# Kernel tuning notes

Measured on AMD Instinct MI355X. Metric: run time of the kernel, lower is better.

Reference implementation:

```python
import jax, jax.numpy as jnp
import numpy as np

D_MODEL = 1024
NUM_HEADS = 16
HEAD_DIM = D_MODEL // NUM_HEADS  # 64


def setup_inputs() -> dict:
    key = jax.random.key(0)
    ks = jax.random.split(key, 9)
    s = 1.0 / np.sqrt(D_MODEL)
    return {
        "x": jax.random.normal(ks[0], (2, 2048, D_MODEL), dtype=jnp.float32),
        "Wq": jax.random.normal(ks[1], (D_MODEL, D_MODEL), dtype=jnp.float32) * s,
        "bq": jnp.zeros((D_MODEL,), dtype=jnp.float32),
        "Wk": jax.random.normal(ks[2], (D_MODEL, HEAD_DIM), dtype=jnp.float32) * s,
        "bk": jnp.zeros((HEAD_DIM,), dtype=jnp.float32),
        "Wv": jax.random.normal(ks[3], (D_MODEL, HEAD_DIM), dtype=jnp.float32) * s,
        "bv": jnp.zeros((HEAD_DIM,), dtype=jnp.float32),
        "Wo": jax.random.normal(ks[4], (D_MODEL, D_MODEL), dtype=jnp.float32) * s,
        "bo": jnp.zeros((D_MODEL,), dtype=jnp.float32),
    }


def reference(x, Wq, bq, Wk, bk, Wv, bv, Wo, bo):
    B, S, D = x.shape
    H, hd = NUM_HEADS, HEAD_DIM
    # Projections: Q has H heads, K/V a single shared head (MQA).
    Q = (x @ Wq + bq).reshape(B, S, H, hd).transpose(0, 2, 1, 3)  # [B,H,S,hd]
    K = x @ Wk + bk  # [B,S,hd]
    V = x @ Wv + bv  # [B,S,hd]
    # Shared-K/V attention: broadcast K across heads instead of expand().
    scores = jnp.einsum("bhqd,bkd->bhqk", Q, K) / np.sqrt(hd)  # [B,H,S,S]
    attn = jax.nn.softmax(scores, axis=-1)
    attended = jnp.einsum("bhqk,bkd->bhqd", attn, V)  # [B,H,S,hd]
    attended = attended.transpose(0, 2, 1, 3).reshape(B, S, D)
    return attended @ Wo + bo
```

## Files before the change

kernel.cpp:

```cpp
#include <hip/hip_runtime.h>
#include <hip/hip_bf16.h>

#define D_MODEL 1024
#define NHEADS  16
#define HD      64
#define BATCH   2
#define SEQ     2048
#define MROWS   4096
#define NQKV    1152
#define NSPLIT  2

typedef short  short4v __attribute__((ext_vector_type(4)));
typedef short  short8  __attribute__((ext_vector_type(8)));
typedef float  floatx4 __attribute__((ext_vector_type(4)));

__device__ inline short f2bf(float f) {
  unsigned u = __builtin_bit_cast(unsigned, f);
  u = (u + 0x7FFF + ((u >> 16) & 1)) >> 16;
  return (short)u;
}

__device__ inline unsigned pack_trunc(float lo, float hi) {
  return __builtin_amdgcn_perm(__builtin_bit_cast(unsigned, hi),
                               __builtin_bit_cast(unsigned, lo), 0x07060302u);
}

__device__ inline void async_copy16(const short* g, short* l) {
  __builtin_amdgcn_global_load_lds(
      (const __attribute__((address_space(1))) unsigned int*)g,
      (__attribute__((address_space(3))) unsigned int*)l, 16, 0, 0);
}

__global__ __launch_bounds__(256)
void prep_kernel(const float* __restrict__ x,  const float* __restrict__ Wq,
                 const float* __restrict__ Wk, const float* __restrict__ Wv,
                 const float* __restrict__ Wo, const float* __restrict__ bq,
                 const float* __restrict__ bk, const float* __restrict__ bv,
                 short* __restrict__ xb, short* __restrict__ Wqkv_t,
                 short* __restrict__ Wo_t, float* __restrict__ bqkv) {
  const int id = blockIdx.x;
  const int t  = threadIdx.x;
  if (id < 544) {
    __shared__ short Ts[64 * 72];
    const float* src; short* dst; int N, off, tile;
    if (id < 256)      { src = Wq; dst = Wqkv_t; N = 1024; off = 0;    tile = id; }
    else if (id < 272) { src = Wk; dst = Wqkv_t; N = 64;   off = 1024; tile = id - 256; }
    else if (id < 288) { src = Wv; dst = Wqkv_t; N = 64;   off = 1088; tile = id - 272; }
    else               { src = Wo; dst = Wo_t;   N = 1024; off = 0;    tile = id - 288; }
    const int k0 = (N == 1024) ? (tile & 15) * 64 : tile * 64;
    const int n0 = (N == 1024) ? (tile >> 4) * 64 : 0;
    {
      const int r = t >> 2, c = (t & 3) * 16;
      const float* s = src + (size_t)(k0 + r) * N + n0 + c;
#pragma unroll
      for (int j = 0; j < 16; j += 4) {
        float4 v = *reinterpret_cast<const float4*>(s + j);
        Ts[r * 72 + c + j + 0] = f2bf(v.x); Ts[r * 72 + c + j + 1] = f2bf(v.y);
        Ts[r * 72 + c + j + 2] = f2bf(v.z); Ts[r * 72 + c + j + 3] = f2bf(v.w);
      }
    }
    __syncthreads();
    {
      const int n = t >> 2, kc = (t & 3) * 16;
      short8 o0, o1;
#pragma unroll
      for (int j = 0; j < 8; ++j) o0[j] = Ts[(kc + j) * 72 + n];
#pragma unroll
      for (int j = 0; j < 8; ++j) o1[j] = Ts[(kc + 8 + j) * 72 + n];
      short* d = dst + (size_t)(off + n0 + n) * 1024 + k0 + kc;
      *reinterpret_cast<short8*>(d)     = o0;
      *reinterpret_cast<short8*>(d + 8) = o1;
    }
  } else if (id < 549) {
    const int i = (id - 544) * 256 + t;
    if (i < 1024)      bqkv[i] = bq[i];
    else if (i < 1088) bqkv[i] = bk[i - 1024];
    else if (i < 1152) bqkv[i] = bv[i - 1088];
  } else {
    const int i = ((id - 549) * 256 + t) * 8;
    if (i < MROWS * D_MODEL) {
      float4 a = *reinterpret_cast<const float4*>(x + i);
      float4 b = *reinterpret_cast<const float4*>(x + i + 4);
      short8 o;
      o[0] = f2bf(a.x); o[1] = f2bf(a.y); o[2] = f2bf(a.z); o[3] = f2bf(a.w);
      o[4] = f2bf(b.x); o[5] = f2bf(b.y); o[6] = f2bf(b.z); o[7] = f2bf(b.w);
      *reinterpret_cast<short8*>(xb + i) = o;
    }
  }
}

template<bool OUT_BF16, int SCALE_N, bool VT_FUSE>
__global__ __launch_bounds__(256)
void gemm_mfma_bt(const short* __restrict__ A, const short* __restrict__ Bt,
                  const float* __restrict__ bias, void* __restrict__ Cout,
                  short* __restrict__ Vtg, int M, int N, int K) {
  __shared__ short As[128 * 64];
  __shared__ short Bs[64 * 64];
  const int t    = threadIdx.x;
  const int w    = t >> 6;
  const int lane = t & 63;
  const int quad = lane >> 4;
  const int l16  = lane & 15;
  const int bm   = blockIdx.x * 128;
  const int bn   = blockIdx.y * 64;
  const int wm   = (w >> 1) * 64;
  const int wn   = (w & 1) * 32;

  const int srow = t >> 3;
  const int cc   = ((t & 7) ^ (srow & 7)) * 8;
  const short* gA = A  + (size_t)(bm + srow) * K + cc;
  const short* gB = Bt + (size_t)(bn + srow) * K + cc;
  short* lA = As + t * 8;
  short* lB = Bs + t * 8;

  floatx4 acc[4][2];
#pragma unroll
  for (int i = 0; i < 4; ++i)
#pragma unroll
    for (int j = 0; j < 2; ++j) acc[i][j] = (floatx4){0.f, 0.f, 0.f, 0.f};

  const int xr = l16 & 7;

  for (int k0 = 0; k0 < K; k0 += 64) {
    __syncthreads();
    async_copy16(gA + k0, lA);
    async_copy16(gA + (size_t)32 * K + k0, lA + 2048);
    async_copy16(gA + (size_t)64 * K + k0, lA + 4096);
    async_copy16(gA + (size_t)96 * K + k0, lA + 6144);
    async_copy16(gB + k0, lB);
    async_copy16(gB + (size_t)32 * K + k0, lB + 2048);
    __syncthreads();

    short8 fa0[4], fa1[4], fb0[2], fb1[2];
#pragma unroll
    for (int mi = 0; mi < 4; ++mi) {
      const int row = wm + mi * 16 + l16;
      fa0[mi] = *reinterpret_cast<const short8*>(&As[row * 64 + (quad ^ xr) * 8]);
      fa1[mi] = *reinterpret_cast<const short8*>(&As[row * 64 + ((4 + quad) ^ xr) * 8]);
    }
#pragma unroll
    for (int ni = 0; ni < 2; ++ni) {
      const int row = wn + ni * 16 + l16;
      fb0[ni] = *reinterpret_cast<const short8*>(&Bs[row * 64 + (quad ^ xr) * 8]);
      fb1[ni] = *reinterpret_cast<const short8*>(&Bs[row * 64 + ((4 + quad) ^ xr) * 8]);
    }
#pragma unroll
    for (int mi = 0; mi < 4; ++mi)
#pragma unroll
      for (int ni = 0; ni < 2; ++ni) {
        acc[mi][ni] = __builtin_amdgcn_mfma_f32_16x16x32_bf16(fa0[mi], fb0[ni], acc[mi][ni], 0, 0, 0);
        acc[mi][ni] = __builtin_amdgcn_mfma_f32_16x16x32_bf16(fa1[mi], fb1[ni], acc[mi][ni], 0, 0, 0);
      }
  }

#pragma unroll
  for (int ni = 0; ni < 2; ++ni) {
    const int col = bn + wn + ni * 16 + l16;
    const float bs = bias[col];
    const float sc = (col < SCALE_N) ? 0.18033688f : 1.0f;
#pragma unroll
    for (int mi = 0; mi < 4; ++mi) {
      const int row = bm + wm + mi * 16 + quad * 4;
      short4v vt4;
#pragma unroll
      for (int r = 0; r < 4; ++r) {
        const float v = (acc[mi][ni][r] + bs) * sc;
        if (OUT_BF16) {
          const short bv16 = f2bf(v);
          ((short*)Cout)[(size_t)(row + r) * N + col] = bv16;
          if (VT_FUSE) vt4[r] = bv16;
        } else {
          ((float*)Cout)[(size_t)(row + r) * N + col] = v;
        }
      }
      if (VT_FUSE && col >= 1088) {
        const int d = col - 1088;
        const int b = row >> 11, s = row & 2047;
        *reinterpret_cast<short4v*>(&Vtg[(size_t)(b * 64 + d) * SEQ + s]) = vt4;
      }
    }
  }
}

__global__ __launch_bounds__(256, 3)
void mqa_flash_bf16(const short* __restrict__ QKV, const short* __restrict__ Vtg,
                    _Float16* __restrict__ Opart, float* __restrict__ lpart) {
  const int bh    = blockIdx.y;
  const int b     = bh >> 4;
  const int h     = bh & 15;
  const int s0    = blockIdx.x * 128;
  const int split = blockIdx.z;
  const int t     = threadIdx.x;
  const int w     = t >> 6;
  const int lane  = t & 63;
  const int quad  = lane >> 4;
  const int l16   = lane & 15;

  __shared__ short KVs[16384];
  __shared__ short Ps[4 * 16 * 72];
  short* myPs = Ps + w * 16 * 72;

  short8 aq[2][2];
#pragma unroll
  for (int st = 0; st < 2; ++st) {
    const short* qrow = &QKV[(size_t)(b * SEQ + s0 + w * 32 + st * 16 + l16) * NQKV + h * HD];
    aq[st][0] = *reinterpret_cast<const short8*>(qrow + quad * 8);
    aq[st][1] = *reinterpret_cast<const short8*>(qrow + 32 + quad * 8);
  }

  floatx4 oacc[2][4];
  floatx4 lacc[2];
#pragma unroll
  for (int st = 0; st < 2; ++st) {
    lacc[st] = (floatx4){0.f, 0.f, 0.f, 0.f};
#pragma unroll
    for (int dg = 0; dg < 4; ++dg) oacc[st][dg] = (floatx4){0.f, 0.f, 0.f, 0.f};
  }

  short8 ones;
#pragma unroll
  for (int j = 0; j < 8; ++j) ones[j] = (short)0x3F80;

  const int srow = t >> 3;
  const int cc   = ((t & 7) ^ (srow & 7)) * 8;
  const short* gK0 = QKV + (size_t)(b * SEQ + srow) * NQKV + 1024 + cc;
  const short* gK1 = gK0 + (size_t)32 * NQKV;
  const short* gV0 = Vtg + (size_t)(b * 64 + srow) * SEQ + cc;
  const short* gV1 = gV0 + (size_t)32 * SEQ;
  short* lK0 = KVs + w * 512;
  short* lK1 = KVs + 2048 + w * 512;
  short* lV0 = KVs + 8192 + w * 512;
  short* lV1 = KVs + 10240 + w * 512;

  const int xr = l16 & 7;
  const int kbase = split * (SEQ / NSPLIT);

  for (int kk = kbase; kk < kbase + SEQ / NSPLIT; kk += 128) {
    __syncthreads();
    async_copy16(gK0 + (size_t)kk * NQKV, lK0);
    async_copy16(gK1 + (size_t)kk * NQKV, lK1);
    async_copy16(gK0 + (size_t)(kk + 64) * NQKV, lK0 + 4096);
    async_copy16(gK1 + (size_t)(kk + 64) * NQKV, lK1 + 4096);
    async_copy16(gV0 + kk, lV0);
    async_copy16(gV1 + kk, lV1);
    async_copy16(gV0 + kk + 64, lV0 + 4096);
    async_copy16(gV1 + kk + 64, lV1 + 4096);
    __syncthreads();

#pragma unroll
    for (int half = 0; half < 2; ++half) {
      const short* Ks = KVs + half * 4096;
      const short* Vt = KVs + 8192 + half * 4096;

      short8 kb[4][2], vb[4][2];
#pragma unroll
      for (int kg = 0; kg < 4; ++kg) {
        kb[kg][0] = *reinterpret_cast<const short8*>(&Ks[(kg * 16 + l16) * 64 + (quad ^ xr) * 8]);
        kb[kg][1] = *reinterpret_cast<const short8*>(&Ks[(kg * 16 + l16) * 64 + ((4 + quad) ^ xr) * 8]);
      }
#pragma unroll
      for (int dg = 0; dg < 4; ++dg) {
        vb[dg][0] = *reinterpret_cast<const short8*>(&Vt[(dg * 16 + l16) * 64 + (quad ^ xr) * 8]);
        vb[dg][1] = *reinterpret_cast<const short8*>(&Vt[(dg * 16 + l16) * 64 + ((4 + quad) ^ xr) * 8]);
      }

#pragma unroll
      for (int st = 0; st < 2; ++st) {
#pragma unroll
        for (int kg = 0; kg < 4; ++kg) {
          floatx4 s4 = (floatx4){0.f, 0.f, 0.f, 0.f};
          s4 = __builtin_amdgcn_mfma_f32_16x16x32_bf16(kb[kg][0], aq[st][0], s4, 0, 0, 0);
          s4 = __builtin_amdgcn_mfma_f32_16x16x32_bf16(kb[kg][1], aq[st][1], s4, 0, 0, 0);
          float p0 = __builtin_exp2f(s4[0]);
          float p1 = __builtin_exp2f(s4[1]);
          float p2 = __builtin_exp2f(s4[2]);
          float p3 = __builtin_exp2f(s4[3]);
          uint2 pk;
          pk.x = pack_trunc(p0, p1);
          pk.y = pack_trunc(p2, p3);
          *reinterpret_cast<uint2*>(&myPs[l16 * 72 + kg * 16 + quad * 4]) = pk;
        }
        short8 ap0 = *reinterpret_cast<const short8*>(&myPs[l16 * 72 + quad * 8]);
        short8 ap1 = *reinterpret_cast<const short8*>(&myPs[l16 * 72 + 32 + quad * 8]);
        lacc[st] = __builtin_amdgcn_mfma_f32_16x16x32_bf16(ap0, ones, lacc[st], 0, 0, 0);
        lacc[st] = __builtin_amdgcn_mfma_f32_16x16x32_bf16(ap1, ones, lacc[st], 0, 0, 0);
#pragma unroll
        for (int dg = 0; dg < 4; ++dg) {
          oacc[st][dg] = __builtin_amdgcn_mfma_f32_16x16x32_bf16(ap0, vb[dg][0], oacc[st][dg], 0, 0, 0);
          oacc[st][dg] = __builtin_amdgcn_mfma_f32_16x16x32_bf16(ap1, vb[dg][1], oacc[st][dg], 0, 0, 0);
        }
      }
    }
  }

#pragma unroll
  for (int st = 0; st < 2; ++st) {
#pragma unroll
    for (int rg = 0; rg < 4; ++rg) {
      const int qg = s0 + w * 32 + st * 16 + quad * 4 + rg;
      _Float16* dst = Opart + ((size_t)(split * 32 + bh) * SEQ + qg) * 64 + l16;
#pragma unroll
      for (int dg = 0; dg < 4; ++dg) dst[dg * 16] = (_Float16)oacc[st][dg][rg];
      if (l16 == 0) lpart[(size_t)(split * 32 + bh) * SEQ + qg] = lacc[st][rg];
    }
  }
}

__global__ __launch_bounds__(256)
void combine_kernel(const _Float16* __restrict__ Opart, const float* __restrict__ lpart,
                    short* __restrict__ Att) {
  const int idx = blockIdx.x * 256 + threadIdx.x;
  const int r   = idx >> 3;
  const int d0  = (idx & 7) * 8;
  float l = 0.f;
  float o[8] = {0.f,0.f,0.f,0.f,0.f,0.f,0.f,0.f};
#pragma unroll
  for (int s = 0; s < NSPLIT; ++s) {
    const _Float16* op = Opart + ((size_t)(s * 32 * SEQ) + r) * 64 + d0;
    l += lpart[(size_t)s * 32 * SEQ + r];
#pragma unroll
    for (int j = 0; j < 8; ++j) o[j] += (float)op[j];
  }
  const float inv = 1.0f / l;
  short8 ov;
#pragma unroll
  for (int j = 0; j < 8; ++j) ov[j] = f2bf(o[j] * inv);
  const int bhh = r >> 11, q = r & 2047;
  const int bb = bhh >> 4, hh = bhh & 15;
  *reinterpret_cast<short8*>(&Att[(size_t)(bb * SEQ + q) * D_MODEL + hh * HD + d0]) = ov;
}

extern "C" void kernel_launch(void* const* d_in, const int* in_sizes, int n_in,
                              void* d_out, int out_size, void* d_ws, size_t ws_size,
                              hipStream_t stream) {
  const float* x  = (const float*)d_in[0];
  const float* Wq = (const float*)d_in[1];
  const float* bq = (const float*)d_in[2];
  const float* Wk = (const float*)d_in[3];
  const float* bk = (const float*)d_in[4];
  const float* Wv = (const float*)d_in[5];
  const float* bv = (const float*)d_in[6];
  const float* Wo = (const float*)d_in[7];
  const float* bo = (const float*)d_in[8];
  float* out = (float*)d_out;

  short* Wqkv_t = (short*)d_ws;
  short* Wo_t   = Wqkv_t + (size_t)NQKV * D_MODEL;
  short* xb     = Wo_t + (size_t)D_MODEL * D_MODEL;
  short* QKV    = xb + (size_t)MROWS * D_MODEL;
  short* Att    = QKV + (size_t)MROWS * NQKV;
  short* Vtg    = Att + (size_t)MROWS * D_MODEL;
  float* bqkv   = (float*)(Vtg + (size_t)BATCH * HD * SEQ);
  float* lpart  = bqkv + 1152;
  _Float16* Opart = (_Float16*)(lpart + (size_t)NSPLIT * 32 * SEQ);

  prep_kernel<<<2597, 256, 0, stream>>>(x, Wq, Wk, Wv, Wo, bq, bk, bv,
                                        xb, Wqkv_t, Wo_t, bqkv);

  gemm_mfma_bt<true, 1024, true><<<dim3(MROWS / 128, NQKV / 64), 256, 0, stream>>>(
      xb, Wqkv_t, bqkv, QKV, Vtg, MROWS, NQKV, D_MODEL);

  mqa_flash_bf16<<<dim3(SEQ / 128, BATCH * NHEADS, NSPLIT), 256, 0, stream>>>(
      QKV, Vtg, Opart, lpart);

  combine_kernel<<<2048, 256, 0, stream>>>(Opart, lpart, Att);

  gemm_mfma_bt<false, 0, false><<<dim3(MROWS / 128, D_MODEL / 64), 256, 0, stream>>>(
      Att, Wo_t, bo, out, nullptr, MROWS, D_MODEL, D_MODEL);
}
```

Baseline: 181.5 us.

## Double-buffer K/V tiles in MQA attention and widen GEMM tiles to 128x128

The attention kernel now processes 64-key tiles with two LDS buffers, prefetching the next tile asynchronously while the current one is computed. This replaces the old scheme of two barriers around each 128-key load and is meant to hide global load latency. The P scratch buffer uses an XOR swizzle instead of padding to avoid bank conflicts, and MFMA sections are raised in priority, with occupancy bumped to 4 blocks. The GEMMs move from 128x64 to 128x128 tiles for more operand reuse per block, at the cost of more registers and fewer blocks in the grid.

```diff
diff --git a/kernel.cpp b/kernel.cpp
--- a/kernel.cpp
+++ b/kernel.cpp
@@ -95,16 +95,16 @@
                   const float* __restrict__ bias, void* __restrict__ Cout,
                   short* __restrict__ Vtg, int M, int N, int K) {
   __shared__ short As[128 * 64];
-  __shared__ short Bs[64 * 64];
+  __shared__ short Bs[128 * 64];
   const int t    = threadIdx.x;
   const int w    = t >> 6;
   const int lane = t & 63;
   const int quad = lane >> 4;
   const int l16  = lane & 15;
   const int bm   = blockIdx.x * 128;
-  const int bn   = blockIdx.y * 64;
+  const int bn   = blockIdx.y * 128;
   const int wm   = (w >> 1) * 64;
-  const int wn   = (w & 1) * 32;
+  const int wn   = (w & 1) * 64;
 
   const int srow = t >> 3;
   const int cc   = ((t & 7) ^ (srow & 7)) * 8;
@@ -113,11 +113,11 @@
   short* lA = As + t * 8;
   short* lB = Bs + t * 8;
 
-  floatx4 acc[4][2];
+  floatx4 acc[4][4];
 #pragma unroll
   for (int i = 0; i < 4; ++i)
 #pragma unroll
-    for (int j = 0; j < 2; ++j) acc[i][j] = (floatx4){0.f, 0.f, 0.f, 0.f};
+    for (int j = 0; j < 4; ++j) acc[i][j] = (floatx4){0.f, 0.f, 0.f, 0.f};
 
   const int xr = l16 & 7;
 
@@ -129,9 +129,11 @@
     async_copy16(gA + (size_t)96 * K + k0, lA + 6144);
     async_copy16(gB + k0, lB);
     async_copy16(gB + (size_t)32 * K + k0, lB + 2048);
+    async_copy16(gB + (size_t)64 * K + k0, lB + 4096);
+    async_copy16(gB + (size_t)96 * K + k0, lB + 6144);
     __syncthreads();
 
-    short8 fa0[4], fa1[4], fb0[2], fb1[2];
+    short8 fa0[4], fa1[4], fb0[4], fb1[4];
 #pragma unroll
     for (int mi = 0; mi < 4; ++mi) {
       const int row = wm + mi * 16 + l16;
@@ -139,7 +141,7 @@
       fa1[mi] = *reinterpret_cast<const short8*>(&As[row * 64 + ((4 + quad) ^ xr) * 8]);
     }
 #pragma unroll
-    for (int ni = 0; ni < 2; ++ni) {
+    for (int ni = 0; ni < 4; ++ni) {
       const int row = wn + ni * 16 + l16;
       fb0[ni] = *reinterpret_cast<const short8*>(&Bs[row * 64 + (quad ^ xr) * 8]);
       fb1[ni] = *reinterpret_cast<const short8*>(&Bs[row * 64 + ((4 + quad) ^ xr) * 8]);
@@ -147,14 +149,14 @@
 #pragma unroll
     for (int mi = 0; mi < 4; ++mi)
 #pragma unroll
-      for (int ni = 0; ni < 2; ++ni) {
+      for (int ni = 0; ni < 4; ++ni) {
         acc[mi][ni] = __builtin_amdgcn_mfma_f32_16x16x32_bf16(fa0[mi], fb0[ni], acc[mi][ni], 0, 0, 0);
         acc[mi][ni] = __builtin_amdgcn_mfma_f32_16x16x32_bf16(fa1[mi], fb1[ni], acc[mi][ni], 0, 0, 0);
       }
   }
 
 #pragma unroll
-  for (int ni = 0; ni < 2; ++ni) {
+  for (int ni = 0; ni < 4; ++ni) {
     const int col = bn + wn + ni * 16 + l16;
     const float bs = bias[col];
     const float sc = (col < SCALE_N) ? 0.18033688f : 1.0f;
@@ -182,7 +184,7 @@
   }
 }
 
-__global__ __launch_bounds__(256, 3)
+__global__ __launch_bounds__(256, 4)
 void mqa_flash_bf16(const short* __restrict__ QKV, const short* __restrict__ Vtg,
                     _Float16* __restrict__ Opart, float* __restrict__ lpart) {
   const int bh    = blockIdx.y;
@@ -197,8 +199,8 @@
   const int l16   = lane & 15;
 
   __shared__ short KVs[16384];
-  __shared__ short Ps[4 * 16 * 72];
-  short* myPs = Ps + w * 16 * 72;
+  __shared__ short Ps[4 * 16 * 64];
+  short* myPs = Ps + w * 1024;
 
   short8 aq[2][2];
 #pragma unroll
@@ -221,76 +223,88 @@
 #pragma unroll
   for (int j = 0; j < 8; ++j) ones[j] = (short)0x3F80;
 
-  const int srow = t >> 3;
-  const int cc   = ((t & 7) ^ (srow & 7)) * 8;
-  const short* gK0 = QKV + (size_t)(b * SEQ + srow) * NQKV + 1024 + cc;
-  const short* gK1 = gK0 + (size_t)32 * NQKV;
-  const short* gV0 = Vtg + (size_t)(b * 64 + srow) * SEQ + cc;
-  const short* gV1 = gV0 + (size_t)32 * SEQ;
-  short* lK0 = KVs + w * 512;
-  short* lK1 = KVs + 2048 + w * 512;
-  short* lV0 = KVs + 8192 + w * 512;
-  short* lV1 = KVs + 10240 + w * 512;
+  const int srow  = t >> 3;
+  const int cc    = ((t & 7) ^ (srow & 7)) * 8;
+  const int kbase = split * (SEQ / NSPLIT);
+  const short* gK = QKV + (size_t)(b * SEQ + kbase + srow) * NQKV + 1024 + cc;
+  const short* gV = Vtg + (size_t)(b * 64 + srow) * SEQ + kbase + cc;
+  short* lK = KVs + w * 512;
+  short* lV = KVs + 4096 + w * 512;
 
   const int xr = l16 & 7;
-  const int kbase = split * (SEQ / NSPLIT);
-
-  for (int kk = kbase; kk < kbase + SEQ / NSPLIT; kk += 128) {
-    __syncthreads();
-    async_copy16(gK0 + (size_t)kk * NQKV, lK0);
-    async_copy16(gK1 + (size_t)kk * NQKV, lK1);
-    async_copy16(gK0 + (size_t)(kk + 64) * NQKV, lK0 + 4096);
-    async_copy16(gK1 + (size_t)(kk + 64) * NQKV, lK1 + 4096);
-    async_copy16(gV0 + kk, lV0);
-    async_copy16(gV1 + kk, lV1);
-    async_copy16(gV0 + kk + 64, lV0 + 4096);
-    async_copy16(gV1 + kk + 64, lV1 + 4096);
-    __syncthreads();
-
-#pragma unroll
-    for (int half = 0; half < 2; ++half) {
-      const short* Ks = KVs + half * 4096;
-      const short* Vt = KVs + 8192 + half * 4096;
-
-      short8 kb[4][2], vb[4][2];
+
+  async_copy16(gK, lK);
+  async_copy16(gK + (size_t)32 * NQKV, lK + 2048);
+  async_copy16(gV, lV);
+  async_copy16(gV + (size_t)32 * SEQ, lV + 2048);
+  gK += (size_t)64 * NQKV;
+  gV += 64;
+
+  const int NT = (SEQ / NSPLIT) / 64;
+  int cur = 0;
+
+  for (int it = 0; it < NT; ++it) {
+    asm volatile("s_waitcnt vmcnt(0)" ::: "memory");
+    __builtin_amdgcn_s_barrier();
+    __builtin_amdgcn_sched_barrier(0);
+
+    if (it + 1 < NT) {
+      const int nb = (cur ^ 1) * 8192;
+      async_copy16(gK, lK + nb);
+      async_copy16(gK + (size_t)32 * NQKV, lK + nb + 2048);
+      async_copy16(gV, lV + nb);
+      async_copy16(gV + (size_t)32 * SEQ, lV + nb + 2048);
+      gK += (size_t)64 * NQKV;
+      gV += 64;
+    }
+
+    const short* Ks = KVs + cur * 8192;
+    const short* Vt = Ks + 4096;
+
+    short8 kb[4][2], vb[4][2];
+#pragma unroll
+    for (int kg = 0; kg < 4; ++kg) {
+      kb[kg][0] = *reinterpret_cast<const short8*>(&Ks[(kg * 16 + l16) * 64 + (quad ^ xr) * 8]);
+      kb[kg][1] = *reinterpret_cast<const short8*>(&Ks[(kg * 16 + l16) * 64 + ((4 + quad) ^ xr) * 8]);
+    }
+#pragma unroll
+    for (int dg = 0; dg < 4; ++dg) {
+      vb[dg][0] = *reinterpret_cast<const short8*>(&Vt[(dg * 16 + l16) * 64 + (quad ^ xr) * 8]);
+      vb[dg][1] = *reinterpret_cast<const short8*>(&Vt[(dg * 16 + l16) * 64 + ((4 + quad) ^ xr) * 8]);
+    }
+    asm volatile("s_waitcnt lgkmcnt(0)" ::: "memory");
+    __builtin_amdgcn_sched_barrier(0);
+
+#pragma unroll
+    for (int st = 0; st < 2; ++st) {
 #pragma unroll
       for (int kg = 0; kg < 4; ++kg) {
-        kb[kg][0] = *reinterpret_cast<const short8*>(&Ks[(kg * 16 + l16) * 64 + (quad ^ xr) * 8]);
-        kb[kg][1] = *reinterpret_cast<const short8*>(&Ks[(kg * 16 + l16) * 64 + ((4 + quad) ^ xr) * 8]);
-      }
+        floatx4 s4 = (floatx4){0.f, 0.f, 0.f, 0.f};
+        s4 = __builtin_amdgcn_mfma_f32_16x16x32_bf16(kb[kg][0], aq[st][0], s4, 0, 0, 0);
+        s4 = __builtin_amdgcn_mfma_f32_16x16x32_bf16(kb[kg][1], aq[st][1], s4, 0, 0, 0);
+        float p0 = __builtin_exp2f(s4[0]);
+        float p1 = __builtin_exp2f(s4[1]);
+        float p2 = __builtin_exp2f(s4[2]);
+        float p3 = __builtin_exp2f(s4[3]);
+        uint2 pk;
+        pk.x = pack_trunc(p0, p1);
+        pk.y = pack_trunc(p2, p3);
+        *reinterpret_cast<uint2*>(
+            &myPs[l16 * 64 + (((2 * kg + (quad >> 1)) ^ xr) * 8) + (quad & 1) * 4]) = pk;
+      }
+      short8 ap0 = *reinterpret_cast<const short8*>(&myPs[l16 * 64 + ((quad ^ xr) * 8)]);
+      short8 ap1 = *reinterpret_cast<const short8*>(&myPs[l16 * 64 + (((4 + quad) ^ xr) * 8)]);
+      __builtin_amdgcn_s_setprio(1);
+      lacc[st] = __builtin_amdgcn_mfma_f32_16x16x32_bf16(ap0, ones, lacc[st], 0, 0, 0);
+      lacc[st] = __builtin_amdgcn_mfma_f32_16x16x32_bf16(ap1, ones, lacc[st], 0, 0, 0);
 #pragma unroll
       for (int dg = 0; dg < 4; ++dg) {
-        vb[dg][0] = *reinterpret_cast<const short8*>(&Vt[(dg * 16 + l16) * 64 + (quad ^ xr) * 8]);
-        vb[dg][1] = *reinterpret_cast<const short8*>(&Vt[(dg * 16 + l16) * 64 + ((4 + quad) ^ xr) * 8]);
-      }
-
-#pragma unroll
-      for (int st = 0; st < 2; ++st) {
-#pragma unroll
-        for (int kg = 0; kg < 4; ++kg) {
-          floatx4 s4 = (floatx4){0.f, 0.f, 0.f, 0.f};
-          s4 = __builtin_amdgcn_mfma_f32_16x16x32_bf16(kb[kg][0], aq[st][0], s4, 0, 0, 0);
-          s4 = __builtin_amdgcn_mfma_f32_16x16x32_bf16(kb[kg][1], aq[st][1], s4, 0, 0, 0);
-          float p0 = __builtin_exp2f(s4[0]);
-          float p1 = __builtin_exp2f(s4[1]);
-          float p2 = __builtin_exp2f(s4[2]);
-          float p3 = __builtin_exp2f(s4[3]);
-          uint2 pk;
-          pk.x = pack_trunc(p0, p1);
-          pk.y = pack_trunc(p2, p3);
-          *reinterpret_cast<uint2*>(&myPs[l16 * 72 + kg * 16 + quad * 4]) = pk;
-        }
-        short8 ap0 = *reinterpret_cast<const short8*>(&myPs[l16 * 72 + quad * 8]);
-        short8 ap1 = *reinterpret_cast<const short8*>(&myPs[l16 * 72 + 32 + quad * 8]);
-        lacc[st] = __builtin_amdgcn_mfma_f32_16x16x32_bf16(ap0, ones, lacc[st], 0, 0, 0);
-        lacc[st] = __builtin_amdgcn_mfma_f32_16x16x32_bf16(ap1, ones, lacc[st], 0, 0, 0);
-#pragma unroll
-        for (int dg = 0; dg < 4; ++dg) {
-          oacc[st][dg] = __builtin_amdgcn_mfma_f32_16x16x32_bf16(ap0, vb[dg][0], oacc[st][dg], 0, 0, 0);
-          oacc[st][dg] = __builtin_amdgcn_mfma_f32_16x16x32_bf16(ap1, vb[dg][1], oacc[st][dg], 0, 0, 0);
-        }
-      }
-    }
+        oacc[st][dg] = __builtin_amdgcn_mfma_f32_16x16x32_bf16(ap0, vb[dg][0], oacc[st][dg], 0, 0, 0);
+        oacc[st][dg] = __builtin_amdgcn_mfma_f32_16x16x32_bf16(ap1, vb[dg][1], oacc[st][dg], 0, 0, 0);
+      }
+      __builtin_amdgcn_s_setprio(0);
+    }
+    cur ^= 1;
   }
 
 #pragma unroll
@@ -357,7 +371,7 @@
   prep_kernel<<<2597, 256, 0, stream>>>(x, Wq, Wk, Wv, Wo, bq, bk, bv,
                                         xb, Wqkv_t, Wo_t, bqkv);
 
-  gemm_mfma_bt<true, 1024, true><<<dim3(MROWS / 128, NQKV / 64), 256, 0, stream>>>(
+  gemm_mfma_bt<true, 1024, true><<<dim3(MROWS / 128, NQKV / 128), 256, 0, stream>>>(
       xb, Wqkv_t, bqkv, QKV, Vtg, MROWS, NQKV, D_MODEL);
 
   mqa_flash_bf16<<<dim3(SEQ / 128, BATCH * NHEADS, NSPLIT), 256, 0, stream>>>(
@@ -365,6 +379,6 @@
 
   combine_kernel<<<2048, 256, 0, stream>>>(Opart, lpart, Att);
 
-  gemm_mfma_bt<false, 0, false><<<dim3(MROWS / 128, D_MODEL / 64), 256, 0, stream>>>(
+  gemm_mfma_bt<false, 0, false><<<dim3(MROWS / 128, D_MODEL / 128), 256, 0, stream>>>(
       Att, Wo_t, bo, out, nullptr, MROWS, D_MODEL, D_MODEL);
 }
```

Result: slower. 241.5 us (+33.1%).
